# Kernel optimization log

Measured on AMD Instinct MI355X. Metric: run time of the kernel, lower is better.

## Reference

```python
import jax, jax.numpy as jnp
import numpy as np

V = 78864; E = 300; H = 512; A = 300; T = 20; DEC_EMB = 512; START = 2


def _pos_encoding(n, d):
    pos = np.arange(n)[:, None].astype(np.float32)
    i = np.arange(d)[None, :]
    angle = pos / np.power(10000.0, (2 * (i // 2)).astype(np.float32) / d)
    pe = np.where(i % 2 == 0, np.sin(angle), np.cos(angle)).astype(np.float32)
    return jnp.asarray(pe)  # [n, d]


def _lstm_cell(x, h, c, Wih, Whh, b):
    g = x @ Wih.T + h @ Whh.T + b
    i, f, gg, o = jnp.split(g, 4, axis=-1)
    c = jax.nn.sigmoid(f) * c + jax.nn.sigmoid(i) * jnp.tanh(gg)
    h = jax.nn.sigmoid(o) * jnp.tanh(c)
    return h, c


def setup_inputs() -> dict:
    key = jax.random.key(0)
    ks = iter(jax.random.split(key, 48))
    B, L = 40, 1000
    def w(shape, s=0.02):
        return jax.random.normal(next(ks), shape, jnp.float32) * s
    def z(shape):
        return jnp.zeros(shape, jnp.float32)
    inp = dict(
        enc_in=jax.random.randint(next(ks), (B, L), 0, V),
        enc_out=jax.random.normal(next(ks), (B, L, H), jnp.float32),
        enc_mask=jnp.zeros((B, L), bool),
        inputs=jax.random.randint(next(ks), (B, T), 0, V),
        embed=w((V, E)),
        elmo1_Wih=w((4 * H, E)), elmo1_Whh=w((4 * H, H)), elmo1_b=z((4 * H,)),
        elmo2_Wih=w((4 * H, H)), elmo2_Whh=w((4 * H, H)), elmo2_b=z((4 * H,)),
        in_W=w((DEC_EMB, H + E + A + H)), in_b=z((DEC_EMB,)),
        rnn1_Wih=w((4 * H, DEC_EMB)), rnn1_Whh=w((4 * H, H)), rnn1_b=z((4 * H,)),
        att1_Wq=w((A, H)), att1_bq=z((A,)), att1_Wk=w((A, H)), att1_bk=z((A,)), att1_Wv=w((A, H)), att1_bv=z((A,)),
        rnn2_Wih=w((4 * H, A)), rnn2_Whh=w((4 * H, H)), rnn2_b=z((4 * H,)),
        att2_Wq=w((A, H)), att2_bq=z((A,)), att2_Wk=w((A, H)), att2_bk=z((A,)), att2_Wv=w((A, H)), att2_bv=z((A,)),
        copy_W=w((A, H)), copy_b=z((A,)),
        out_W=w((V, A)), out_b=z((V,)),
        scale=jnp.asarray(1.0, jnp.float32),
    )
    return inp


def _forward(enc_in, enc_out, enc_mask, inputs, embed,
             elmo1_Wih, elmo1_Whh, elmo1_b, elmo2_Wih, elmo2_Whh, elmo2_b,
             in_W, in_b, rnn1_Wih, rnn1_Whh, rnn1_b,
             att1_Wq, att1_bq, att1_Wk, att1_bk, att1_Wv, att1_bv,
             rnn2_Wih, rnn2_Whh, rnn2_b,
             att2_Wq, att2_bq, att2_Wk, att2_bk, att2_Wv, att2_bv,
             copy_W, copy_b, out_W, out_b, scale):
    B, L = enc_in.shape
    pe = _pos_encoding(T, DEC_EMB)  # [T, 512]
    # Precompute per-encoder projections (hoisted out of the step loop).
    K1 = jnp.einsum('blh,ah->bla', enc_out, att1_Wk) + att1_bk
    V1 = jnp.einsum('blh,ah->bla', enc_out, att1_Wv) + att1_bv
    K2 = jnp.einsum('blh,ah->bla', enc_out, att2_Wk) + att2_bk
    V2 = jnp.einsum('blh,ah->bla', enc_out, att2_Wv) + att2_bv
    copyK = jnp.tanh(jnp.einsum('blh,ah->bla', enc_out, copy_W) + copy_b)
    bidx = jnp.arange(B)[:, None]

    def attn(h, Wq, bq, K, Vp):
        q = h @ Wq.T + bq                          # [B, A]
        s = jnp.einsum('ba,bla->bl', q, K)
        s = jnp.where(enc_mask, -1e9, s)
        p = jax.nn.softmax(s, axis=-1)
        return jnp.einsum('bl,bla->ba', p, Vp)

    # teacher forcing with random_int=0 -> always use ground-truth inputs
    sym_in = jnp.concatenate([jnp.full((B, 1), START, inputs.dtype), inputs[:, :-1]], axis=1).T  # [T,B]
    sym_out = inputs.T  # [T,B]

    zf = lambda *s: jnp.zeros(s, enc_out.dtype)
    carry0 = (zf(B, H), zf(B, H), zf(B, H), zf(B, H),  # elmo h1,c1,h2,c2
              zf(B, H), zf(B, H), zf(B, H), zf(B, H),  # rnn1 h,c ; rnn2 h,c
              zf(B, A), zf(B, H))                       # dec_att_out, select_read

    def step(carry, xs):
        eh1, ec1, eh2, ec2, h1, c1, h2, c2, att, sel = carry
        pe_t, s_in, s_out = xs
        emb = embed[s_in]                                           # [B, E]
        eh1, ec1 = _lstm_cell(emb, eh1, ec1, elmo1_Wih, elmo1_Whh, elmo1_b)
        eh2, ec2 = _lstm_cell(eh1, eh2, ec2, elmo2_Wih, elmo2_Whh, elmo2_b)
        in_embed = jnp.concatenate([emb, eh2], axis=-1)              # [B, 812]
        dec_in = jnp.concatenate([in_embed, att, sel], axis=-1) @ in_W.T + in_b + pe_t
        h1, c1 = _lstm_cell(dec_in, h1, c1, rnn1_Wih, rnn1_Whh, rnn1_b)
        att = attn(h1, att1_Wq, att1_bq, K1, V1)
        h2, c2 = _lstm_cell(att, h2, c2, rnn2_Wih, rnn2_Whh, rnn2_b)
        att = attn(h2, att2_Wq, att2_bq, K2, V2) + att
        # copy scores
        s = jnp.einsum('ba,bla->bl', att, copyK)
        s = jnp.where(enc_mask, -1e9, s)
        score_c = jax.nn.softmax(s, axis=-1)
        score_e = score_c * scale * scale
        vocab = att @ out_W.T + out_b                                # [B, V]
        vocab = vocab.at[bidx, enc_in].add(score_e)
        sym_pred = jnp.argmax(vocab, axis=-1).astype(jnp.int32)
        eq = (enc_in == s_out[:, None]).astype(score_c.dtype)
        score_f = score_c * eq
        score_f = score_f / (jnp.sum(score_f, axis=-1, keepdims=True) + 1e-8)
        sel = jnp.einsum('bl,blh->bh', score_f, enc_out)
        return (eh1, ec1, eh2, ec2, h1, c1, h2, c2, att, sel), (vocab, sym_pred)

    _, (dec_out, syms) = jax.lax.scan(step, carry0, (pe, sym_in, sym_out))
    return jnp.transpose(dec_out, (1, 0, 2)), syms.T  # [B,T,V], [B,T]


def reference(enc_in, enc_out, enc_mask, inputs, embed,
              elmo1_Wih, elmo1_Whh, elmo1_b, elmo2_Wih, elmo2_Whh, elmo2_b,
              in_W, in_b, rnn1_Wih, rnn1_Whh, rnn1_b,
              att1_Wq, att1_bq, att1_Wk, att1_bk, att1_Wv, att1_bv,
              rnn2_Wih, rnn2_Whh, rnn2_b,
              att2_Wq, att2_bq, att2_Wk, att2_bk, att2_Wv, att2_bv,
              copy_W, copy_b, out_W, out_b, scale):
    return _forward(enc_in, enc_out, enc_mask, inputs, embed,
                    elmo1_Wih, elmo1_Whh, elmo1_b, elmo2_Wih, elmo2_Whh, elmo2_b,
                    in_W, in_b, rnn1_Wih, rnn1_Whh, rnn1_b,
                    att1_Wq, att1_bq, att1_Wk, att1_bk, att1_Wv, att1_bv,
                    rnn2_Wih, rnn2_Whh, rnn2_b,
                    att2_Wq, att2_bq, att2_Wk, att2_bk, att2_Wv, att2_bv,
                    copy_W, copy_b, out_W, out_b, scale)
```

## Files before the change

### kernel.cpp

```cpp
#include <hip/hip_runtime.h>
#include <math.h>

#define B_ 40
#define L_ 1000
#define H_ 512
#define A_ 300
#define T_ 20
#define E_ 300
#define V_ 78864
#define START_ 2

#define NBLK 256
#define NTHR 512
#define NVT 309

#define OFF_CKH   0ul
#define OFF_M1T   6400000ul
#define OFF_M2T   6662144ul
#define OFF_BQK1  6924288ul
#define OFF_BQK2  6924800ul
#define OFF_QK    6925312ul
#define OFF_DEC   6945792ul
#define OFF_ATT1  6966272ul
#define OFF_CPART 6978272ul
#define OFF_CSTAT 7101152ul
#define OFF_ATTA  7101632ul
#define OFF_SCCA  7341632ul
#define OFF_STT   8141632ul
#define OFF_ATT2  8469312ul
#define OFF_SELP  8481312ul
#define OFF_CNT   8604192ul
#define WS_END    8604256ul

struct P {
  const int* enc_in; const float* enc; const unsigned char* mask; const int* inputs;
  const float* embed;
  const float *e1Wih,*e1Whh,*e1b,*e2Wih,*e2Whh,*e2b;
  const float *inW,*inb;
  const float *r1Wih,*r1Whh,*r1b;
  const float *a1Wq,*a1bq,*a1Wk,*a1Wv,*a1bv;
  const float *r2Wih,*r2Whh,*r2b;
  const float *a2Wq,*a2bq,*a2Wk,*a2Wv,*a2bv;
  const float *cW,*cb,*oW,*ob,*scale;
  float* dout;
  unsigned short* copyKh;
  float *M1T,*M2T,*bqk1,*bqk2,*qk,*dec,*att1,*cpart,*cstat,*attTall,*sccAll,*stt,*att2,*selp;
  unsigned* cnt;
};

__device__ __forceinline__ float sigm(float x){ return 1.0f/(1.0f+expf(-x)); }

__device__ __forceinline__ float wredSum(float v){
#pragma unroll
  for(int o=32;o>0;o>>=1) v+=__shfl_xor(v,o);
  return v;
}
__device__ __forceinline__ float wredMax(float v){
#pragma unroll
  for(int o=32;o>0;o>>=1) v=fmaxf(v,__shfl_xor(v,o));
  return v;
}
__device__ __forceinline__ unsigned short f2bf(float f){
  unsigned u=__float_as_uint(f);
  u=(u+0x7fffu+((u>>16)&1u))>>16;
  return (unsigned short)u;
}

__device__ __forceinline__ void gbar(unsigned* cnt, unsigned target){
  __syncthreads();
  if(threadIdx.x==0){
    __hip_atomic_fetch_add(cnt,1u,__ATOMIC_RELEASE,__HIP_MEMORY_SCOPE_AGENT);
    while(__hip_atomic_load(cnt,__ATOMIC_RELAXED,__HIP_MEMORY_SCOPE_AGENT)<target){
      __builtin_amdgcn_s_sleep(1);
    }
    (void)__hip_atomic_load(cnt,__ATOMIC_ACQUIRE,__HIP_MEMORY_SCOPE_AGENT);
  }
  __syncthreads();
}

template<typename SRC>
static __device__ __forceinline__ void gv_accum(float* xs,int K,const float* Wrow,
    float& acc,int lane,int kq,int nq,SRC src){
  for(int k0=0;k0<K;k0+=256){
    int ch=min(256,K-k0);
    __syncthreads();
    if(ch==256){
      float r[20];
#pragma unroll
      for(int u=0;u<20;u++){
        int i=threadIdx.x+u*NTHR;
        r[u]=src(i>>8,k0+(i&255));
      }
#pragma unroll
      for(int u=0;u<20;u++){
        int i=threadIdx.x+u*NTHR;
        xs[(i>>8)*257+(i&255)]=r[u];
      }
    } else {
      for(int i=threadIdx.x;i<40*ch;i+=NTHR){
        int bb=i/ch, kk=i-bb*ch;
        xs[bb*257+kk]=src(bb,k0+kk);
      }
    }
    __syncthreads();
    if(lane<40){
      float a0=0.f,a1=0.f,a2=0.f,a3=0.f;
      int k=kq;
      for(;k+3*nq<ch;k+=4*nq){
        a0+=Wrow[k0+k     ]*xs[lane*257+k];
        a1+=Wrow[k0+k+  nq]*xs[lane*257+k+  nq];
        a2+=Wrow[k0+k+2*nq]*xs[lane*257+k+2*nq];
        a3+=Wrow[k0+k+3*nq]*xs[lane*257+k+3*nq];
      }
      for(;k<ch;k+=nq) a0+=Wrow[k0+k]*xs[lane*257+k];
      acc+=a0+a1+a2+a3;
    }
  }
}

static __device__ void lstm_ph(const P& p,float* SH,float* gld,int t,
    const float* Wih,int XD,const float* Whh,const float* bias,
    const float* xvec,bool gather,
    const float* hr,const float* cr,float* hw,float* cw){
  int tid=threadIdx.x,w=tid>>6,lane=tid&63;
  int gate=w&3,usub=w>>2;
  int row=gate*H_+(blockIdx.x*2+usub);
  int rowu=__builtin_amdgcn_readfirstlane(row);
  float acc=bias[rowu];
  const float* W1=Wih+(size_t)rowu*XD;
  if(gather){
    const int* inp=p.inputs; const float* emb=p.embed; int tt=t;
    gv_accum(SH,XD,W1,acc,lane,0,1,[=](int bb,int kk)->float{
      int si=(tt==0)?START_:inp[bb*T_+tt-1];
      return emb[(size_t)si*E_+kk];});
  }else{
    gv_accum(SH,XD,W1,acc,lane,0,1,[=](int bb,int kk)->float{
      return xvec[(size_t)bb*XD+kk];});
  }
  const float* W2=Whh+(size_t)rowu*H_;
  gv_accum(SH,H_,W2,acc,lane,0,1,[=](int bb,int kk)->float{
    return hr[bb*H_+kk];});
  gld[w*64+lane]=acc;
  __syncthreads();
  if(w<2&&lane<40){
    int u=blockIdx.x*2+w,b=lane;
    float gi=gld[(w*4+0)*64+b],gf=gld[(w*4+1)*64+b],gg=gld[(w*4+2)*64+b],go=gld[(w*4+3)*64+b];
    float c=cr[b*H_+u];
    float cn=sigm(gf)*c+sigm(gi)*tanhf(gg);
    hw[b*H_+u]=sigm(go)*tanhf(cn);
    cw[b*H_+u]=cn;
  }
  __syncthreads();
}

static __device__ void qk_ph(const P& p,float* SH,const float* hsrc,
    const float* MT,const float* bqk){
  int tid=threadIdx.x;
  if(blockIdx.x>=240) return;
  int b=blockIdx.x/6, j=blockIdx.x%6;
  SH[tid]=hsrc[b*H_+tid];
  __syncthreads();
  int h0=j*86, hc=min(86,H_-h0);
  if(tid<hc){
    int hp=h0+tid;
    float a=bqk[hp];
    const float4* mr=(const float4*)(MT+(size_t)hp*H_);
#pragma unroll 8
    for(int i=0;i<H_/4;i++){
      float4 m4=mr[i];
      a+=SH[4*i]*m4.x+SH[4*i+1]*m4.y+SH[4*i+2]*m4.z+SH[4*i+3]*m4.w;
    }
    p.qk[b*H_+hp]=a;
  }
}

static __device__ void scctx_ph(const P& p,float* SH){
  int tid=threadIdx.x,w=tid>>6,lane=tid&63;
  if(blockIdx.x>=240) return;
  int b=blockIdx.x/6, j=blockIdx.x%6;
  int l0=j*167, lcnt=min(167,L_-l0);
  const float* qrow=p.qk+b*H_;
  float4 q0=*(const float4*)(qrow+lane*8);
  float4 q1=*(const float4*)(qrow+lane*8+4);
  float* tile=SH;
  float* sc16=SH+8192;
  const float4* base=(const float4*)(p.enc+((size_t)(b*L_+l0))*H_);
  float4 pre[4];
  { int rem=lcnt*128;
#pragma unroll
    for(int u=0;u<4;u++){ int i=tid+u*NTHR; pre[u]=(i<rem)?base[i]:make_float4(0.f,0.f,0.f,0.f); } }
  float m=-3.0e38f,S=0.f,acc=0.f;
  for(int t0=0;t0<lcnt;t0+=16){
    int tc=min(16,lcnt-t0);
    __syncthreads();
    { float4* dst=(float4*)tile;
#pragma unroll
      for(int u=0;u<4;u++){ int i=tid+u*NTHR; if(i<tc*128) dst[i]=pre[u]; } }
    __syncthreads();
    if(t0+16<lcnt){
      int rem=(lcnt-t0-16)*128;
      const float4* src=base+(size_t)(t0+16)*128;
#pragma unroll
      for(int u=0;u<4;u++){ int i=tid+u*NTHR; pre[u]=(i<rem)?src[i]:make_float4(0.f,0.f,0.f,0.f); }
    }
#pragma unroll
    for(int r=0;r<2;r++){
      int row=w*2+r;
      float sc=-1e30f;
      if(row<tc){
        const float4* er=(const float4*)(tile+row*512);
        float4 e0=er[lane*2], e1=er[lane*2+1];
        float pp=q0.x*e0.x+q0.y*e0.y+q0.z*e0.z+q0.w*e0.w
                +q1.x*e1.x+q1.y*e1.y+q1.z*e1.z+q1.w*e1.w;
        pp=wredSum(pp);
        sc=p.mask[b*L_+l0+t0+row]?-1e9f:pp;
      }
      if(lane==0) sc16[row]=sc;
    }
    __syncthreads();
    float tm=-3.0e38f;
    for(int r=0;r<tc;r++) tm=fmaxf(tm,sc16[r]);
    float mn=fmaxf(m,tm);
    float scl=expf(m-mn);
    float Sadd=0.f, aadd=0.f;
    for(int r=0;r<tc;r++){
      float pe=expf(sc16[r]-mn);
      Sadd+=pe;
      aadd+=pe*tile[r*512+tid];
    }
    S=S*scl+Sadd;
    acc=acc*scl+aadd;
    m=mn;
  }
  p.cpart[(size_t)(b*6+j)*H_+tid]=acc;
  if(tid==0){p.cstat[(b*6+j)*2]=m; p.cstat[(b*6+j)*2+1]=S;}
}

static __device__ void atto_ph(const P& p,float* SH,const float* Wv,const float* bv,
    bool ADD,int t){
  int tid=threadIdx.x;
  if(blockIdx.x>=40) return;
  int b=blockIdx.x;
  float mb=-3.0e38f;
#pragma unroll
  for(int j=0;j<6;j++) mb=fmaxf(mb,p.cstat[(b*6+j)*2]);
  float Sb=0.f;
#pragma unroll
  for(int j=0;j<6;j++) Sb+=p.cstat[(b*6+j)*2+1]*expf(p.cstat[(b*6+j)*2]-mb);
  float inv=1.0f/Sb;
  float cx=0.f;
#pragma unroll
  for(int j=0;j<6;j++) cx+=expf(p.cstat[(b*6+j)*2]-mb)*p.cpart[(size_t)(b*6+j)*H_+tid];
  SH[tid]=cx*inv;
  __syncthreads();
  if(tid<A_){
    float a=bv[tid];
    const float4* wr=(const float4*)(Wv+(size_t)tid*H_);
#pragma unroll 8
    for(int i=0;i<H_/4;i++){
      float4 w4=wr[i];
      a+=SH[4*i]*w4.x+SH[4*i+1]*w4.y+SH[4*i+2]*w4.z+SH[4*i+3]*w4.w;
    }
    if(ADD){
      a+=p.att1[b*A_+tid];
      p.att2[b*A_+tid]=a;
      p.attTall[(size_t)t*A_*B_+tid*B_+b]=a;
    }
    else p.att1[b*A_+tid]=a;
  }
}

static __device__ void copysc_ph(const P& p,int t){
  int tid=threadIdx.x,w=tid>>6,lane=tid&63;
  if(blockIdx.x>=240) return;
  int b=blockIdx.x/6, j=blockIdx.x%6;
  int l0=j*167, lcnt=min(167,L_-l0);
  float* scct=p.sccAll+(size_t)t*B_*L_;
  float ar[8];
#pragma unroll
  for(int q=0;q<8;q++){
    int a=lane*8+q;
    ar[q]=(lane<40&&a<A_)? p.att2[b*A_+a] : 0.f;
  }
  for(int l=l0+w;l<l0+lcnt;l+=8){
    float pp=0.f;
    if(lane<40){
      const uint4* cr=(const uint4*)(p.copyKh+((size_t)(b*L_+l))*320);
      uint4 kk=cr[lane];
      pp =ar[0]*__uint_as_float(kk.x<<16)+ar[1]*__uint_as_float(kk.x&0xffff0000u);
      pp+=ar[2]*__uint_as_float(kk.y<<16)+ar[3]*__uint_as_float(kk.y&0xffff0000u);
      pp+=ar[4]*__uint_as_float(kk.z<<16)+ar[5]*__uint_as_float(kk.z&0xffff0000u);
      pp+=ar[6]*__uint_as_float(kk.w<<16)+ar[7]*__uint_as_float(kk.w&0xffff0000u);
    }
    pp=wredSum(pp);
    if(lane==0) scct[b*L_+l]=p.mask[b*L_+l]?-1e9f:pp;
  }
}

static __device__ void sel_ph(const P& p,float* SH,float* red,int t){
  int tid=threadIdx.x,w=tid>>6,lane=tid&63;
  if(blockIdx.x>=240) return;
  int b=blockIdx.x/6, j=blockIdx.x%6;
  int l0=j*167, lcnt=min(167,L_-l0);
  const float* scct=p.sccAll+(size_t)t*B_*L_;
  for(int i=tid;i<L_;i+=NTHR) SH[i]=scct[b*L_+i];
  __syncthreads();
  float lm=-3.0e38f;
  for(int i=tid;i<L_;i+=NTHR) lm=fmaxf(lm,SH[i]);
  lm=wredMax(lm);
  if(lane==0) red[w]=lm;
  __syncthreads();
  float m=red[0];
#pragma unroll
  for(int q=1;q<8;q++) m=fmaxf(m,red[q]);
  __syncthreads();
  int so=p.inputs[b*T_+t];
  float ls=0.f,lq=0.f;
  for(int i=tid;i<L_;i+=NTHR){
    float exv=expf(SH[i]-m);
    ls+=exv;
    if(p.enc_in[b*L_+i]==so) lq+=exv;
  }
  ls=wredSum(ls); lq=wredSum(lq);
  if(lane==0){red[w]=ls; red[8+w]=lq;}
  __syncthreads();
  float S=0.f,Q=0.f;
#pragma unroll
  for(int q=0;q<8;q++){S+=red[q];Q+=red[8+q];}
  if(tid<lcnt){
    int l=l0+tid;
    float exv=expf(SH[l]-m);
    SH[1024+tid]=(p.enc_in[b*L_+l]==so)?exv:0.f;
  }
  __syncthreads();
  int h4=tid&127, rg=tid>>7;
  float4 a4=make_float4(0.f,0.f,0.f,0.f);
#pragma unroll 2
  for(int li=rg;li<lcnt;li+=4){
    float wgt=SH[1024+li];
    float4 ev=*(const float4*)(p.enc+((size_t)(b*L_+l0+li))*H_+h4*4);
    a4.x+=wgt*ev.x; a4.y+=wgt*ev.y; a4.z+=wgt*ev.z; a4.w+=wgt*ev.w;
  }
  *(float4*)(SH+2048+tid*4)=a4;
  __syncthreads();
  float inv=1.0f/(Q+1e-8f*S);
  float s=SH[2048+tid]+SH[2048+512+tid]+SH[2048+1024+tid]+SH[2048+1536+tid];
  p.selp[(size_t)(b*6+j)*H_+tid]=s*inv;
}

__global__ __launch_bounds__(NTHR,2) void k_persist(P p){
  __shared__ float SH[10560];
  __shared__ float gld[512];
  __shared__ float red[16];
  int blk=blockIdx.x, tid=threadIdx.x;
  unsigned bt=0;
#define BARR() do{bt++; gbar(p.cnt,bt*(unsigned)NBLK);}while(0)

  {
    int mm=blk>>7, r0=(blk&127)*4;
    const float* Wq = mm? p.a2Wq : p.a1Wq;
    const float* Wk = mm? p.a2Wk : p.a1Wk;
    float* MT = mm? p.M2T : p.M1T;
    float s0=0.f,s1=0.f,s2=0.f,s3=0.f;
    for(int a=0;a<A_;a++){
      float wq=Wq[a*H_+tid];
      s0+=wq*Wk[a*H_+r0+0];
      s1+=wq*Wk[a*H_+r0+1];
      s2+=wq*Wk[a*H_+r0+2];
      s3+=wq*Wk[a*H_+r0+3];
    }
    MT[(size_t)(r0+0)*H_+tid]=s0;
    MT[(size_t)(r0+1)*H_+tid]=s1;
    MT[(size_t)(r0+2)*H_+tid]=s2;
    MT[(size_t)(r0+3)*H_+tid]=s3;
    if((blk&127)==0){
      const float* bq = mm? p.a2bq : p.a1bq;
      float ab=0.f;
      for(int a=0;a<A_;a++) ab+=bq[a]*Wk[a*H_+tid];
      (mm? p.bqk2 : p.bqk1)[tid]=ab;
    }
  }
  for(int item=blk;item<B_*63;item+=NBLK){
    int b=item/63, lt=item-b*63;
    int l0=lt*16, lcnt=min(16,L_-l0);
    float acc[16];
    float bv=(tid<A_)?p.cb[tid]:0.f;
#pragma unroll
    for(int l=0;l<16;l++) acc[l]=bv;
    for(int k0=0;k0<H_;k0+=32){
      __syncthreads();
      for(int i=tid;i<A_*32;i+=NTHR){
        int a=i>>5,kc=i&31;
        SH[a*33+kc]=p.cW[(size_t)a*H_+k0+kc];
      }
      __syncthreads();
      if(tid<A_){
#pragma unroll
        for(int l=0;l<16;l++){
          if(l<lcnt){
            const float* es=p.enc+((size_t)(b*L_+l0+l))*H_+k0;
            float al=acc[l];
#pragma unroll
            for(int kc=0;kc<32;kc++) al+=SH[tid*33+kc]*es[kc];
            acc[l]=al;
          }
        }
      }
    }
    if(tid<320){
#pragma unroll
      for(int l=0;l<16;l++){
        if(l<lcnt){
          unsigned short hv=0;
          if(tid<A_) hv=f2bf(tanhf(acc[l]));
          p.copyKh[((size_t)(b*L_+l0+l))*320+tid]=hv;
        }
      }
    }
  }
  BARR();

  for(int t=0;t<T_;t++){
    int rp=t&1, wp=rp^1;
    float* stt=p.stt;
    auto SL=[&](int i,int par){ return stt+((size_t)(i*2+par))*(B_*H_); };
    float *eh1r=SL(0,rp),*eh1w=SL(0,wp),*ec1r=SL(1,rp),*ec1w=SL(1,wp);
    float *eh2r=SL(2,rp),*eh2w=SL(2,wp),*ec2r=SL(3,rp),*ec2w=SL(3,wp);
    float *h1r=SL(4,rp),*h1w=SL(4,wp),*c1r=SL(5,rp),*c1w=SL(5,wp);
    float *h2r=SL(6,rp),*h2w=SL(6,wp),*c2r=SL(7,rp),*c2w=SL(7,wp);

    lstm_ph(p,SH,gld,t,p.e1Wih,E_,p.e1Whh,p.e1b,nullptr,true ,eh1r,ec1r,eh1w,ec1w); BARR();
    lstm_ph(p,SH,gld,t,p.e2Wih,H_,p.e2Whh,p.e2b,eh1w  ,false,eh2r,ec2r,eh2w,ec2w); BARR();

    {
      int w=tid>>6,lane=tid&63;
      int usub=w>>2, kq=w&3;
      int unit=blk*2+usub;
      int rowu=__builtin_amdgcn_readfirstlane(unit);
      float acc=0.f;
      const float* Wr=p.inW+(size_t)rowu*1624;
      const int* inp=p.inputs; const float* emb=p.embed;
      const float* e2=eh2w; const float* a2c=p.att2; const float* sp=p.selp;
      int tt=t;
      gv_accum(SH,1624,Wr,acc,lane,kq,4,[=](int bb,int kk)->float{
        if(kk<E_){int si=(tt==0)?START_:inp[bb*T_+tt-1];return emb[(size_t)si*E_+kk];}
        else if(kk<E_+H_) return e2[bb*H_+kk-E_];
        else if(kk<E_+H_+A_) return a2c[bb*A_+kk-(E_+H_)];
        else{
          int hh=kk-(E_+H_+A_); float s=0.f;
#pragma unroll
          for(int jj=0;jj<6;jj++) s+=sp[(size_t)(bb*6+jj)*H_+hh];
          return s;
        }
      });
      gld[(usub*4+kq)*64+lane]=acc;
      __syncthreads();
      if(w<2&&lane<40){
        int u=blk*2+w;
        float s=gld[(w*4+0)*64+lane]+gld[(w*4+1)*64+lane]
               +gld[(w*4+2)*64+lane]+gld[(w*4+3)*64+lane];
        float ex=(float)(2*(u>>1))/512.0f;
        float ang=(float)t/powf(10000.0f,ex);
        s+=p.inb[u]+((u&1)?cosf(ang):sinf(ang));
        p.dec[lane*H_+u]=s;
      }
      __syncthreads();
    }
    BARR();

    lstm_ph(p,SH,gld,t,p.r1Wih,H_,p.r1Whh,p.r1b,p.dec ,false,h1r,c1r,h1w,c1w); BARR();
    qk_ph(p,SH,h1w,p.M1T,p.bqk1);                                              BARR();
    scctx_ph(p,SH);                                                            BARR();
    atto_ph(p,SH,p.a1Wv,p.a1bv,false,t);                                       BARR();
    lstm_ph(p,SH,gld,t,p.r2Wih,A_,p.r2Whh,p.r2b,p.att1,false,h2r,c2r,h2w,c2w); BARR();
    qk_ph(p,SH,h2w,p.M2T,p.bqk2);                                              BARR();
    scctx_ph(p,SH);                                                            BARR();
    atto_ph(p,SH,p.a2Wv,p.a2bv,true,t);                                        BARR();
    copysc_ph(p,t);                                                            BARR();
    sel_ph(p,SH,red,t);                                                        BARR();
  }

  {
    int row=tid>>1, half=tid&1;
    for(int item=blk;item<NVT*T_;item+=NBLK){
      int vt=item/T_, t=item-vt*T_;
      long v0=(long)vt*256;
      int vcnt=min(256,(int)(V_-v0));
      float acc[20];
#pragma unroll
      for(int q=0;q<20;q++) acc[q]=0.f;
      for(int c=0;c<10;c++){
        int a0=c*32, aw=min(32,A_-a0);
        __syncthreads();
        if(c<9){
          int tot=vcnt*8;
          for(int i=tid;i<tot;i+=NTHR){
            int vr=i>>3, f=i&7;
            *(float4*)&SH[vr*36+f*4]=*(const float4*)(p.oW+(size_t)(v0+vr)*A_+a0+f*4);
          }
          for(int i=tid;i<32*40;i+=NTHR) SH[9216+i]=p.attTall[(size_t)t*A_*B_+a0*B_+i];
        } else {
          int tot=vcnt*3;
          for(int i=tid;i<tot;i+=NTHR){
            int vr=i/3, f=i-vr*3;
            *(float4*)&SH[vr*36+f*4]=*(const float4*)(p.oW+(size_t)(v0+vr)*A_+a0+f*4);
          }
          for(int i=tid;i<12*40;i+=NTHR) SH[9216+i]=p.attTall[(size_t)t*A_*B_+a0*B_+i];
        }
        __syncthreads();
        if(row<vcnt){
          const float* wrow=&SH[row*36];
          for(int ac=0;ac<aw;ac++){
            float wv=wrow[ac];
            const float* at=&SH[9216+ac*40+half*20];
#pragma unroll
            for(int bq=0;bq<5;bq++){
              float4 t4=*(const float4*)(at+bq*4);
              acc[bq*4+0]+=wv*t4.x; acc[bq*4+1]+=wv*t4.y;
              acc[bq*4+2]+=wv*t4.z; acc[bq*4+3]+=wv*t4.w;
            }
          }
        }
      }
      if(row<vcnt){
        long v=v0+row;
        float obv=p.ob[v];
#pragma unroll
        for(int bb=0;bb<20;bb++){
          int b=half*20+bb;
          p.dout[((size_t)(b*T_+t))*V_+v]=acc[bb]+obv;
        }
      }
    }
  }
  BARR();

  {
    int w=tid>>6,lane=tid&63;
    float sc2=p.scale[0]*p.scale[0];
    for(int it=blk;it<B_*T_;it+=NBLK){
      int b=it/T_, t=it-b*T_;
      const float* scr=p.sccAll+((size_t)t*B_+b)*L_;
      __syncthreads();
      for(int i=tid;i<L_;i+=NTHR) SH[i]=scr[i];
      __syncthreads();
      float lm=-3.0e38f;
      for(int i=tid;i<L_;i+=NTHR) lm=fmaxf(lm,SH[i]);
      lm=wredMax(lm);
      if(lane==0) red[w]=lm;
      __syncthreads();
      float m=red[0];
#pragma unroll
      for(int q=1;q<8;q++) m=fmaxf(m,red[q]);
      __syncthreads();
      float ls=0.f;
      for(int i=tid;i<L_;i+=NTHR) ls+=expf(SH[i]-m);
      ls=wredSum(ls);
      if(lane==0) red[w]=ls;
      __syncthreads();
      float S=0.f;
#pragma unroll
      for(int q=0;q<8;q++) S+=red[q];
      float f=sc2/S;
      float* drow=p.dout+((size_t)(b*T_+t))*V_;
      const int* ei=p.enc_in+b*L_;
      for(int i=tid;i<L_;i+=NTHR) atomicAdd(drow+ei[i], expf(SH[i]-m)*f);
      __syncthreads();
    }
  }
  BARR();

  {
    int* isa=(int*)(SH+512);
    for(int it=blk;it<B_*T_;it+=NBLK){
      int b=it/T_, t=it-b*T_;
      const float* row=p.dout+((size_t)(b*T_+t))*V_;
      float best=-3.0e38f; int bi=0;
      for(int i4=tid;i4<V_/4;i4+=NTHR){
        float4 x=((const float4*)row)[i4];
        int base=i4*4;
        if(x.x>best){best=x.x;bi=base;}
        if(x.y>best){best=x.y;bi=base+1;}
        if(x.z>best){best=x.z;bi=base+2;}
        if(x.w>best){best=x.w;bi=base+3;}
      }
      __syncthreads();
      SH[tid]=best; isa[tid]=bi;
      __syncthreads();
      for(int off=256;off>0;off>>=1){
        if(tid<off){
          float ov=SH[tid+off]; int oi=isa[tid+off];
          if(ov>SH[tid]||(ov==SH[tid]&&oi<isa[tid])){SH[tid]=ov; isa[tid]=oi;}
        }
        __syncthreads();
      }
      if(tid==0) p.dout[(size_t)B_*T_*V_+b*T_+t]=(float)isa[0];
    }
  }
#undef BARR
}

extern "C" void kernel_launch(void* const* d_in, const int* in_sizes, int n_in,
                              void* d_out, int out_size, void* d_ws, size_t ws_size,
                              hipStream_t stream){
  P p;
  p.enc_in=(const int*)d_in[0];
  p.enc   =(const float*)d_in[1];
  p.mask  =(const unsigned char*)d_in[2];
  p.inputs=(const int*)d_in[3];
  p.embed =(const float*)d_in[4];
  p.e1Wih=(const float*)d_in[5];  p.e1Whh=(const float*)d_in[6];  p.e1b=(const float*)d_in[7];
  p.e2Wih=(const float*)d_in[8];  p.e2Whh=(const float*)d_in[9];  p.e2b=(const float*)d_in[10];
  p.inW  =(const float*)d_in[11]; p.inb  =(const float*)d_in[12];
  p.r1Wih=(const float*)d_in[13]; p.r1Whh=(const float*)d_in[14]; p.r1b=(const float*)d_in[15];
  p.a1Wq =(const float*)d_in[16]; p.a1bq =(const float*)d_in[17];
  p.a1Wk =(const float*)d_in[18];
  p.a1Wv =(const float*)d_in[20]; p.a1bv =(const float*)d_in[21];
  p.r2Wih=(const float*)d_in[22]; p.r2Whh=(const float*)d_in[23]; p.r2b=(const float*)d_in[24];
  p.a2Wq =(const float*)d_in[25]; p.a2bq =(const float*)d_in[26];
  p.a2Wk =(const float*)d_in[27];
  p.a2Wv =(const float*)d_in[29]; p.a2bv =(const float*)d_in[30];
  p.cW   =(const float*)d_in[31]; p.cb   =(const float*)d_in[32];
  p.oW   =(const float*)d_in[33]; p.ob   =(const float*)d_in[34];
  p.scale=(const float*)d_in[35];
  p.dout=(float*)d_out;

  float* w=(float*)d_ws;
  p.copyKh=(unsigned short*)(w+OFF_CKH);
  p.M1T  =w+OFF_M1T;    p.M2T =w+OFF_M2T;
  p.bqk1 =w+OFF_BQK1;   p.bqk2=w+OFF_BQK2;
  p.qk   =w+OFF_QK;     p.dec =w+OFF_DEC;
  p.att1 =w+OFF_ATT1;
  p.cpart=w+OFF_CPART;  p.cstat=w+OFF_CSTAT;
  p.attTall=w+OFF_ATTA; p.sccAll=w+OFF_SCCA;
  p.stt  =w+OFF_STT;
  p.att2 =w+OFF_ATT2;   p.selp=w+OFF_SELP;
  p.cnt  =(unsigned*)(w+OFF_CNT);

  hipMemsetAsync(w+OFF_STT,0,(WS_END-OFF_STT)*sizeof(float),stream);
  k_persist<<<NBLK,NTHR,0,stream>>>(p);
}
```

Baseline: 17.38 ms.

## Replace atomic-counter grid barrier with per-block flag barrier; enlarge score tile

```diff
diff --git a/kernel.cpp b/kernel.cpp
--- a/kernel.cpp
+++ b/kernel.cpp
@@ -29,8 +29,9 @@
 #define OFF_STT   8141632ul
 #define OFF_ATT2  8469312ul
 #define OFF_SELP  8481312ul
-#define OFF_CNT   8604192ul
-#define WS_END    8604256ul
+#define OFF_FLAGS 8604192ul
+#define OFF_REL   8612384ul
+#define WS_END    8612448ul
 
 struct P {
   const int* enc_in; const float* enc; const unsigned char* mask; const int* inputs;
@@ -45,7 +46,7 @@
   float* dout;
   unsigned short* copyKh;
   float *M1T,*M2T,*bqk1,*bqk2,*qk,*dec,*att1,*cpart,*cstat,*attTall,*sccAll,*stt,*att2,*selp;
-  unsigned* cnt;
+  unsigned *flags,*rel;
 };
 
 __device__ __forceinline__ float sigm(float x){ return 1.0f/(1.0f+expf(-x)); }
@@ -66,16 +67,27 @@
   return (unsigned short)u;
 }
 
-__device__ __forceinline__ void gbar(unsigned* cnt, unsigned target){
-  __syncthreads();
-  if(threadIdx.x==0){
-    __hip_atomic_fetch_add(cnt,1u,__ATOMIC_RELEASE,__HIP_MEMORY_SCOPE_AGENT);
-    while(__hip_atomic_load(cnt,__ATOMIC_RELAXED,__HIP_MEMORY_SCOPE_AGENT)<target){
-      __builtin_amdgcn_s_sleep(1);
-    }
-    (void)__hip_atomic_load(cnt,__ATOMIC_ACQUIRE,__HIP_MEMORY_SCOPE_AGENT);
-  }
-  __syncthreads();
+__device__ __forceinline__ void gbar2(unsigned* flags, unsigned* rel, unsigned epoch){
+  __syncthreads();
+  int tid=threadIdx.x;
+  if(blockIdx.x==0){
+    if(tid>0 && tid<NBLK){
+      while(__hip_atomic_load(flags+(unsigned)tid*32u,__ATOMIC_RELAXED,__HIP_MEMORY_SCOPE_AGENT)<epoch)
+        __builtin_amdgcn_s_sleep(2);
+      (void)__hip_atomic_load(flags+(unsigned)tid*32u,__ATOMIC_ACQUIRE,__HIP_MEMORY_SCOPE_AGENT);
+    }
+    __syncthreads();
+    if(tid==0)
+      __hip_atomic_store(rel,epoch,__ATOMIC_RELEASE,__HIP_MEMORY_SCOPE_AGENT);
+  } else {
+    if(tid==0){
+      __hip_atomic_store(flags+(unsigned)blockIdx.x*32u,epoch,__ATOMIC_RELEASE,__HIP_MEMORY_SCOPE_AGENT);
+      while(__hip_atomic_load(rel,__ATOMIC_RELAXED,__HIP_MEMORY_SCOPE_AGENT)<epoch)
+        __builtin_amdgcn_s_sleep(2);
+      (void)__hip_atomic_load(rel,__ATOMIC_ACQUIRE,__HIP_MEMORY_SCOPE_AGENT);
+    }
+    __syncthreads();
+  }
 }
 
 template<typename SRC>
@@ -183,29 +195,29 @@
   float4 q0=*(const float4*)(qrow+lane*8);
   float4 q1=*(const float4*)(qrow+lane*8+4);
   float* tile=SH;
-  float* sc16=SH+8192;
+  float* sc24=SH+12288;
   const float4* base=(const float4*)(p.enc+((size_t)(b*L_+l0))*H_);
-  float4 pre[4];
+  float4 pre[6];
   { int rem=lcnt*128;
 #pragma unroll
-    for(int u=0;u<4;u++){ int i=tid+u*NTHR; pre[u]=(i<rem)?base[i]:make_float4(0.f,0.f,0.f,0.f); } }
+    for(int u=0;u<6;u++){ int i=tid+u*NTHR; pre[u]=(i<rem)?base[i]:make_float4(0.f,0.f,0.f,0.f); } }
   float m=-3.0e38f,S=0.f,acc=0.f;
-  for(int t0=0;t0<lcnt;t0+=16){
-    int tc=min(16,lcnt-t0);
+  for(int t0=0;t0<lcnt;t0+=24){
+    int tc=min(24,lcnt-t0);
     __syncthreads();
     { float4* dst=(float4*)tile;
 #pragma unroll
-      for(int u=0;u<4;u++){ int i=tid+u*NTHR; if(i<tc*128) dst[i]=pre[u]; } }
+      for(int u=0;u<6;u++){ int i=tid+u*NTHR; if(i<tc*128) dst[i]=pre[u]; } }
     __syncthreads();
-    if(t0+16<lcnt){
-      int rem=(lcnt-t0-16)*128;
-      const float4* src=base+(size_t)(t0+16)*128;
-#pragma unroll
-      for(int u=0;u<4;u++){ int i=tid+u*NTHR; pre[u]=(i<rem)?src[i]:make_float4(0.f,0.f,0.f,0.f); }
-    }
-#pragma unroll
-    for(int r=0;r<2;r++){
-      int row=w*2+r;
+    if(t0+24<lcnt){
+      int rem=(lcnt-t0-24)*128;
+      const float4* src=base+(size_t)(t0+24)*128;
+#pragma unroll
+      for(int u=0;u<6;u++){ int i=tid+u*NTHR; pre[u]=(i<rem)?src[i]:make_float4(0.f,0.f,0.f,0.f); }
+    }
+#pragma unroll
+    for(int r=0;r<3;r++){
+      int row=w*3+r;
       float sc=-1e30f;
       if(row<tc){
         const float4* er=(const float4*)(tile+row*512);
@@ -215,16 +227,16 @@
         pp=wredSum(pp);
         sc=p.mask[b*L_+l0+t0+row]?-1e9f:pp;
       }
-      if(lane==0) sc16[row]=sc;
+      if(lane==0) sc24[row]=sc;
     }
     __syncthreads();
     float tm=-3.0e38f;
-    for(int r=0;r<tc;r++) tm=fmaxf(tm,sc16[r]);
+    for(int r=0;r<tc;r++) tm=fmaxf(tm,sc24[r]);
     float mn=fmaxf(m,tm);
     float scl=expf(m-mn);
     float Sadd=0.f, aadd=0.f;
     for(int r=0;r<tc;r++){
-      float pe=expf(sc16[r]-mn);
+      float pe=expf(sc24[r]-mn);
       Sadd+=pe;
       aadd+=pe*tile[r*512+tid];
     }
@@ -349,12 +361,12 @@
 }
 
 __global__ __launch_bounds__(NTHR,2) void k_persist(P p){
-  __shared__ float SH[10560];
+  __shared__ float SH[12544];
   __shared__ float gld[512];
   __shared__ float red[16];
   int blk=blockIdx.x, tid=threadIdx.x;
   unsigned bt=0;
-#define BARR() do{bt++; gbar(p.cnt,bt*(unsigned)NBLK);}while(0)
+#define BARR() do{bt++; gbar2(p.flags,p.rel,bt);}while(0)
 
   {
     int mm=blk>>7, r0=(blk&127)*4;
@@ -635,7 +647,8 @@
   p.attTall=w+OFF_ATTA; p.sccAll=w+OFF_SCCA;
   p.stt  =w+OFF_STT;
   p.att2 =w+OFF_ATT2;   p.selp=w+OFF_SELP;
-  p.cnt  =(unsigned*)(w+OFF_CNT);
+  p.flags=(unsigned*)(w+OFF_FLAGS);
+  p.rel  =(unsigned*)(w+OFF_REL);
 
   hipMemsetAsync(w+OFF_STT,0,(WS_END-OFF_STT)*sizeof(float),stream);
   k_persist<<<NBLK,NTHR,0,stream>>>(p);
```

Measured after the change: 16.09 ms. 7.4% less time.
